# Optimization experiments

Hardware: AMD Instinct MI355X
Metric: run time of the kernel (lower is better)

Reference implementation:

```python
import jax, jax.numpy as jnp
import numpy as np

N = 8192          # batch_size == number of graph nodes
F1 = 64
F2 = 64
D_IN = F1 * F2    # 4096, = int(sqrt(in_feats))**2
D_OUT = 4096      # out_feats, must equal F1*F2 for the final reshape
ALPHA = 0.2       # LeakyReLU negative slope


def setup_inputs() -> dict:
    key = jax.random.key(0)
    k_x, k_w, k_a = jax.random.split(key, 3)
    x = jax.random.normal(k_x, (N, F1, F2), dtype=jnp.float32)
    # torch Linear weight layout: [out_feats, in_feats]; xavier-uniform-ish scale
    lim_w = float(np.sqrt(6.0 / (D_IN + D_OUT)) * np.sqrt(2.0))
    W = jax.random.uniform(k_w, (D_OUT, D_IN), dtype=jnp.float32, minval=-lim_w, maxval=lim_w)
    lim_a = float(np.sqrt(6.0 / (1 + 2 * D_OUT)))
    a = jax.random.uniform(k_a, (1, 2 * D_OUT), dtype=jnp.float32, minval=-lim_a, maxval=lim_a)
    return {"x": x, "W": W, "a": a}


def reference(x, W, a):
    b, f1, f2 = x.shape
    x_flat = x.reshape(b, f1 * f2)                 # [N, D_in]
    h = x_flat @ W.T                               # [N, D_out]
    # scores[i,j] = leakyrelu(cat(h_i, h_j) @ a.T) = leakyrelu(h_i.a1 + h_j.a2)
    a1 = a[0, :D_OUT]                              # [D_out]
    a2 = a[0, D_OUT:]                              # [D_out]
    s1 = h @ a1                                    # [N]
    s2 = h @ a2                                    # [N]
    e = s1[:, None] + s2[None, :]                  # [N, N]
    e = jnp.where(e > 0, e, ALPHA * e)             # LeakyReLU
    attention = jax.nn.softmax(e, axis=-1)         # [N, N]
    # dropout=0.0 (eval-mode / deterministic reference)
    out = attention @ h                            # [N, D_out]
    return out.reshape(b, f1, f2)
```

## Files before the change

### kernel.cpp

```cpp
#include <hip/hip_runtime.h>
#include <hip/hip_bf16.h>
#include <stdint.h>


typedef float  f32x4  __attribute__((ext_vector_type(4)));
typedef __bf16 bf16x8 __attribute__((ext_vector_type(8)));

#define AS1 __attribute__((address_space(1)))
#define AS3 __attribute__((address_space(3)))

constexpr int NB  = 8192;
constexpr int DF  = 4096;
constexpr int CH  = 64;
constexpr int NCH = NB / CH;

constexpr int GK  = DF;
constexpr int BKK = 64;
constexpr int NT2 = GK / BKK;

__device__ __forceinline__ uint16_t f2bf_u(float f) {
  union { float f; uint32_t u; } x; x.f = f;
  return (uint16_t)((x.u + 0x7FFFu + ((x.u >> 16) & 1u)) >> 16);
}
__device__ __forceinline__ float bfu2f(uint16_t v) {
  union { uint32_t u; float f; } x; x.u = ((uint32_t)v) << 16;
  return x.f;
}

__global__ __launch_bounds__(256) void cvt_f32_to_bf16(
    const float* __restrict__ in, uint16_t* __restrict__ out, int n4) {
  int idx = blockIdx.x * 256 + threadIdx.x;
  int stride = gridDim.x * 256;
  for (int i = idx; i < n4; i += stride) {
    float4 v = ((const float4*)in)[i];
    ushort4 o;
    o.x = f2bf_u(v.x); o.y = f2bf_u(v.y); o.z = f2bf_u(v.z); o.w = f2bf_u(v.w);
    ((ushort4*)out)[i] = o;
  }
}


#define STAGE_A(tt, half) do {                                                 \
  const uint16_t* g0_ = Ag + (size_t)((half) * 128) * GK + (size_t)(tt) * BKK; \
  uint32_t d_ = ((uint32_t)((tt) & 1)) * 32768u + (uint32_t)(half) * 8192u +   \
                (uint32_t)wave * 512u;                                         \
  __builtin_amdgcn_global_load_lds((const AS1 void*)g0_,                       \
      (AS3 void*)(lds + d_), 16, 0, 0);                                        \
  __builtin_amdgcn_global_load_lds((const AS1 void*)(g0_ + (size_t)64 * GK),   \
      (AS3 void*)(lds + d_ + 4096u), 16, 0, 0);                                \
} while (0)

#define STAGE_B(tt, half) do {                                                 \
  const uint16_t* g0_ = Bg + (size_t)((half) * 128) * GK + (size_t)(tt) * BKK; \
  uint32_t d_ = ((uint32_t)((tt) & 1)) * 32768u + 16384u +                     \
                (uint32_t)(half) * 8192u + (uint32_t)wave * 512u;              \
  __builtin_amdgcn_global_load_lds((const AS1 void*)g0_,                       \
      (AS3 void*)(lds + d_), 16, 0, 0);                                        \
  __builtin_amdgcn_global_load_lds((const AS1 void*)(g0_ + (size_t)64 * GK),   \
      (AS3 void*)(lds + d_ + 4096u), 16, 0, 0);                                \
} while (0)

#define LDA(mh) do {                                                           \
  _Pragma("unroll") for (int mf = 0; mf < 4; ++mf)                             \
    _Pragma("unroll") for (int ks = 0; ks < 2; ++ks)                           \
      aF[mf][ks] = *(const bf16x8*)(lds + bufo +                               \
          (uint32_t)(wm * 128 + (mh) * 64 + mf * 16 + lr) * 64u +              \
          (uint32_t)((ks * 32 + lg * 8) ^ swl));                               \
} while (0)

#define LDB(nh) do {                                                           \
  _Pragma("unroll") for (int nf = 0; nf < 2; ++nf)                             \
    _Pragma("unroll") for (int ks = 0; ks < 2; ++ks)                           \
      bF[nf][ks] = *(const bf16x8*)(lds + bufo + 16384u +                      \
          (uint32_t)(wn * 64 + (nh) * 32 + nf * 16 + lr) * 64u +               \
          (uint32_t)((ks * 32 + lg * 8) ^ swl));                               \
} while (0)

#define MMA(mh, nh) do {                                                       \
  _Pragma("unroll") for (int mf = 0; mf < 4; ++mf)                             \
    _Pragma("unroll") for (int nf = 0; nf < 2; ++nf)                           \
      _Pragma("unroll") for (int ks = 0; ks < 2; ++ks)                         \
        acc[(mh) * 4 + mf][(nh) * 2 + nf] =                                    \
            __builtin_amdgcn_mfma_f32_16x16x32_bf16(aF[mf][ks], bF[nf][ks],    \
                acc[(mh) * 4 + mf][(nh) * 2 + nf], 0, 0, 0);                   \
} while (0)

__global__ __launch_bounds__(512, 2) void gemm_nt_8phase(
    const uint16_t* __restrict__ A, const uint16_t* __restrict__ B,
    uint16_t* __restrict__ C) {
  __shared__ uint16_t lds[65536];

  const int tid  = threadIdx.x;
  const int wave = tid >> 6;
  const int lane = tid & 63;
  const int lr   = lane & 15;
  const int lg   = lane >> 4;
  const int wm   = wave >> 2;
  const int wn   = wave & 3;
  const int swl  = (lr & 7) << 3;

  const int bid = blockIdx.x;
  const int swz = (bid & 7) * 64 + (bid >> 3);
  const int bx  = swz & 15;
  const int by  = swz >> 4;
  const int rowBase = by * 256;
  const int colBase = bx * 256;

  const int sr  = tid >> 3;
  const int sch = (tid & 7) ^ (sr & 7);
  const uint16_t* Ag = A + (size_t)(rowBase + sr) * GK + sch * 8;
  const uint16_t* Bg = B + (size_t)(colBase + sr) * GK + sch * 8;

  f32x4 acc[8][4];
#pragma unroll
  for (int mf = 0; mf < 8; ++mf)
#pragma unroll
    for (int nf = 0; nf < 4; ++nf) acc[mf][nf] = (f32x4){0.f, 0.f, 0.f, 0.f};

  STAGE_A(0, 0);
  STAGE_B(0, 1);
  STAGE_A(0, 1);
  STAGE_B(0, 0);
  STAGE_A(1, 0);
  STAGE_B(1, 1);
  asm volatile("s_waitcnt vmcnt(4)" ::: "memory");
  __builtin_amdgcn_s_barrier();

  bf16x8 aF[4][2], bF[2][2];

  for (int t = 0; t < NT2; ++t) {
    const uint32_t bufo = ((uint32_t)(t & 1)) * 32768u;

    LDA(0); LDB(0);
    if (t + 1 < NT2) STAGE_A(t + 1, 1);
    __builtin_amdgcn_s_barrier();
    __builtin_amdgcn_s_setprio(1);
    MMA(0, 0);
    __builtin_amdgcn_s_setprio(0);
    __builtin_amdgcn_s_barrier();

    LDB(1);
    if (t + 1 < NT2) STAGE_B(t + 1, 0);
    __builtin_amdgcn_s_barrier();
    __builtin_amdgcn_s_setprio(1);
    MMA(0, 1);
    __builtin_amdgcn_s_setprio(0);
    __builtin_amdgcn_s_barrier();

    LDA(1);
    if (t + 2 < NT2) STAGE_A(t + 2, 0);
    __builtin_amdgcn_s_barrier();
    __builtin_amdgcn_s_setprio(1);
    MMA(1, 1);
    __builtin_amdgcn_s_setprio(0);
    __builtin_amdgcn_s_barrier();

    LDB(0);
    if (t + 2 < NT2) STAGE_B(t + 2, 1);
    __builtin_amdgcn_s_barrier();
    __builtin_amdgcn_s_setprio(1);
    MMA(1, 0);
    __builtin_amdgcn_s_setprio(0);
    if (t + 2 < NT2) {
      asm volatile("s_waitcnt vmcnt(4)" ::: "memory");
    } else if (t + 1 < NT2) {
      asm volatile("s_waitcnt vmcnt(0)" ::: "memory");
    }
    __builtin_amdgcn_s_barrier();
  }

  const int r0 = rowBase + wm * 128 + lg * 4;
  const int c0 = colBase + wn * 64 + lr;
#pragma unroll
  for (int mf = 0; mf < 8; ++mf)
#pragma unroll
    for (int nf = 0; nf < 4; ++nf)
#pragma unroll
      for (int e = 0; e < 4; ++e)
        C[(size_t)(r0 + mf * 16 + e) * (size_t)DF + (c0 + nf * 16)] =
            f2bf_u(acc[mf][nf][e]);
}

__global__ __launch_bounds__(256) void s12_kernel(
    const uint16_t* __restrict__ h, const float* __restrict__ a,
    float* __restrict__ s1, float* __restrict__ s2) {
  const int wave = threadIdx.x >> 6, lane = threadIdx.x & 63;
  const int row = blockIdx.x * 4 + wave;
  const uint32_t* hr = (const uint32_t*)(h + (size_t)row * DF);
  float d1 = 0.f, d2 = 0.f;
#pragma unroll 4
  for (int it = 0; it < DF / 128; it++) {
    int u = it * 64 + lane;
    uint32_t hv = hr[u];
    float lo = bfu2f((uint16_t)hv), hi = bfu2f((uint16_t)(hv >> 16));
    int k = 2 * u;
    d1 += a[k] * lo + a[k + 1] * hi;
    d2 += a[DF + k] * lo + a[DF + k + 1] * hi;
  }
  for (int off = 32; off > 0; off >>= 1) {
    d1 += __shfl_down(d1, off, 64);
    d2 += __shfl_down(d2, off, 64);
  }
  if (lane == 0) { s1[row] = d1; s2[row] = d2; }
}

__global__ __launch_bounds__(256) void rank_kernel(
    const float* __restrict__ s2, int* __restrict__ pi,
    float* __restrict__ s2sorted) {
  __shared__ float ld[NB];
  for (int idx = threadIdx.x; idx < NB; idx += 256) ld[idx] = s2[idx];
  __syncthreads();
  const int j = blockIdx.x * 256 + threadIdx.x;
  const float v = ld[j];
  int cnt = 0;
  for (int q = 0; q < NB / 4; q++) {
    float4 u = ((const float4*)ld)[q];
    int jj = q * 4;
    cnt += (u.x > v) || (u.x == v && (jj + 0) < j);
    cnt += (u.y > v) || (u.y == v && (jj + 1) < j);
    cnt += (u.z > v) || (u.z == v && (jj + 2) < j);
    cnt += (u.w > v) || (u.w == v && (jj + 3) < j);
  }
  pi[cnt] = j;
  s2sorted[cnt] = v;
}

__global__ __launch_bounds__(256) void count_kernel(
    const float* __restrict__ s1, const float* __restrict__ s2,
    int* __restrict__ ci) {
  __shared__ float ld[NB];
  for (int idx = threadIdx.x; idx < NB; idx += 256) ld[idx] = s2[idx];
  __syncthreads();
  const int i = blockIdx.x * 256 + threadIdx.x;
  const float thr = -s1[i];
  int cnt = 0;
  for (int q = 0; q < NB / 4; q++) {
    float4 u = ((const float4*)ld)[q];
    cnt += (u.x > thr) + (u.y > thr) + (u.z > thr) + (u.w > thr);
  }
  ci[i] = cnt;
}

__global__ __launch_bounds__(256) void scan_kernel(
    const float* __restrict__ s2sorted, float* __restrict__ Sb,
    float* __restrict__ Sc, float* __restrict__ wbg, float* __restrict__ wcg) {
  __shared__ float pb[256], pc[256];
  const int t = threadIdx.x;
  float sb = 0.f, sc = 0.f;
  for (int c = t * 32; c < t * 32 + 32; c++) {
    float s = s2sorted[c];
    float wb = __expf(0.2f * s), wc = __expf(s);
    wbg[c] = wb; wcg[c] = wc;
    sb += wb; sc += wc;
  }
  pb[t] = sb; pc[t] = sc;
  __syncthreads();
  if (t == 0) {
    float rb = 0.f, rc = 0.f;
    for (int q = 0; q < 256; q++) {
      float tb = pb[q], tc = pc[q];
      pb[q] = rb; pc[q] = rc;
      rb += tb; rc += tc;
    }
    Sb[0] = 0.f; Sc[0] = 0.f;
    Sb[NB] = rb; Sc[NB] = rc;
  }
  __syncthreads();
  float rb = pb[t], rc = pc[t];
  for (int c = t * 32; c < t * 32 + 32; c++) {
    rb += wbg[c]; rc += wcg[c];
    if (c + 1 < NB) { Sb[c + 1] = rb; Sc[c + 1] = rc; }
  }
}

__global__ __launch_bounds__(256) void zero_hist(int* __restrict__ hist) {
  int t = blockIdx.x * 256 + threadIdx.x;
  if (t <= NB) hist[t] = 0;
}

__global__ __launch_bounds__(256) void finalize_kernel(
    const float* __restrict__ s1, const int* __restrict__ ci,
    const float* __restrict__ Sb, const float* __restrict__ Sc,
    float* __restrict__ f1, float* __restrict__ f2, int* __restrict__ hist) {
  const int i = blockIdx.x * 256 + threadIdx.x;
  const float s1i = s1[i];
  const int c = ci[i];
  const float q1 = __expf(0.2f * s1i), q2 = __expf(s1i);
  const float l = q1 * (Sb[NB] - Sb[c]) + q2 * Sc[c];
  f1[i] = q1 / l;
  f2[i] = q2 / l;
  atomicAdd(&hist[c], 1);
}

__global__ __launch_bounds__(256) void bucket_scan(
    const int* __restrict__ hist, int* __restrict__ istart,
    int* __restrict__ cursor) {
  __shared__ int ps[256];
  const int t = threadIdx.x;
  const int lo = t * 33;
  const int hi = min(lo + 33, NB + 1);
  int s = 0;
  for (int b = lo; b < hi; b++) s += hist[b];
  ps[t] = s;
  __syncthreads();
  if (t == 0) {
    int r = 0;
    for (int q = 0; q < 256; q++) { int v = ps[q]; ps[q] = r; r += v; }
  }
  __syncthreads();
  int r = ps[t];
  for (int b = lo; b < hi; b++) { istart[b] = r; cursor[b] = r; r += hist[b]; }
  if (t == 255) istart[NB + 1] = r;
}

__global__ __launch_bounds__(256) void scatter_kernel(
    const int* __restrict__ ci, int* __restrict__ cursor,
    int* __restrict__ ilist) {
  const int i = blockIdx.x * 256 + threadIdx.x;
  const int b = ci[i];
  const int pos = atomicAdd(&cursor[b], 1);
  ilist[pos] = i;
}

__global__ __launch_bounds__(256) void pass1_kernel(
    const uint16_t* __restrict__ h, const int* __restrict__ pi,
    const float* __restrict__ wbg, const float* __restrict__ wcg,
    float* __restrict__ Bct, float* __restrict__ Cct) {
  __shared__ int   pj[CH];
  __shared__ float wb[CH], wc[CH];
  const int t  = threadIdx.x;
  const int cb = blockIdx.x;
  const int k  = blockIdx.y;
  if (t < CH) {
    int g = k * CH + t;
    pj[t] = pi[g]; wb[t] = wbg[g]; wc[t] = wcg[g];
  }
  __syncthreads();
  const int n0 = cb * 512 + t * 2;
  float b0 = 0.f, b1 = 0.f, c0 = 0.f, c1 = 0.f;
#pragma unroll 4
  for (int c = 0; c < CH; c++) {
    uint32_t hv = *(const uint32_t*)(h + (size_t)pj[c] * DF + n0);
    float h0 = bfu2f((uint16_t)hv), h1 = bfu2f((uint16_t)(hv >> 16));
    b0 += wb[c] * h0; b1 += wb[c] * h1;
    c0 += wc[c] * h0; c1 += wc[c] * h1;
  }
  *(float2*)(Bct + (size_t)k * DF + n0) = make_float2(b0, b1);
  *(float2*)(Cct + (size_t)k * DF + n0) = make_float2(c0, c1);
}

__global__ __launch_bounds__(256) void boff_kernel(
    const float* __restrict__ Bct, const float* __restrict__ Cct,
    float* __restrict__ Boff, float* __restrict__ Coff) {
  const int n = blockIdx.x * 256 + threadIdx.x;
  float ob = 0.f, oc = 0.f;
  for (int k = 0; k < NCH; k++) {
    Boff[(size_t)k * DF + n] = ob;
    Coff[(size_t)k * DF + n] = oc;
    ob += Bct[(size_t)k * DF + n];
    oc += Cct[(size_t)k * DF + n];
  }
  Boff[(size_t)NCH * DF + n] = ob;
  Coff[(size_t)NCH * DF + n] = oc;
}

__global__ __launch_bounds__(256) void pass2_kernel(
    const uint16_t* __restrict__ h, const int* __restrict__ pi,
    const float* __restrict__ wbg, const float* __restrict__ wcg,
    const float* __restrict__ Boff, const float* __restrict__ Coff,
    const int* __restrict__ istart, const int* __restrict__ ilist,
    const float* __restrict__ f1, const float* __restrict__ f2,
    float* __restrict__ out) {
  __shared__ int   pj[CH];
  __shared__ float wb[CH], wc[CH];
  __shared__ int   se[CH + 2];
  const int t  = threadIdx.x;
  const int cb = blockIdx.x;
  const int k  = blockIdx.y;
  if (t < CH) {
    int g = k * CH + t;
    pj[t] = pi[g]; wb[t] = wbg[g]; wc[t] = wcg[g];
  }
  if (t < CH + 2) se[t] = istart[k * CH + t];
  __syncthreads();
  const int n0 = cb * 512 + t * 2;
  const float2 An = *(const float2*)(Boff + (size_t)NCH * DF + n0);
  const float2 Bo = *(const float2*)(Boff + (size_t)k * DF + n0);
  const float2 Co = *(const float2*)(Coff + (size_t)k * DF + n0);
  float b0 = Bo.x, b1 = Bo.y, c0 = Co.x, c1 = Co.y;

  if (k == 0) {
    for (int idx = se[0]; idx < se[1]; idx++) {
      const int i = ilist[idx];
      const float fa = f1[i];
      *(float2*)(out + (size_t)i * DF + n0) = make_float2(fa * An.x, fa * An.y);
    }
  }
  for (int c = 0; c < CH; c++) {
    uint32_t hv = *(const uint32_t*)(h + (size_t)pj[c] * DF + n0);
    float h0 = bfu2f((uint16_t)hv), h1 = bfu2f((uint16_t)(hv >> 16));
    b0 += wb[c] * h0; b1 += wb[c] * h1;
    c0 += wc[c] * h0; c1 += wc[c] * h1;
    const int e0 = se[c + 1], e1 = se[c + 2];
    for (int idx = e0; idx < e1; idx++) {
      const int i = ilist[idx];
      const float fa = f1[i], fb = f2[i];
      float o0 = fa * (An.x - b0) + fb * c0;
      float o1 = fa * (An.y - b1) + fb * c1;
      *(float2*)(out + (size_t)i * DF + n0) = make_float2(o0, o1);
    }
  }
}

extern "C" void kernel_launch(void* const* d_in, const int* in_sizes, int n_in,
                              void* d_out, int out_size, void* d_ws, size_t ws_size,
                              hipStream_t stream) {
  const float* x = (const float*)d_in[0];
  const float* W = (const float*)d_in[1];
  const float* a = (const float*)d_in[2];
  float* out = (float*)d_out;

  char* ws = (char*)d_ws;
  uint16_t* h = (uint16_t*)ws;
  char* sm = ws + 67108864;
  float* s1       = (float*)(sm);
  float* s2       = (float*)(sm + 65536);
  float* s2sorted = (float*)(sm + 131072);
  int*   pi       = (int*)  (sm + 196608);
  int*   ci       = (int*)  (sm + 262144);
  float* Sb       = (float*)(sm + 327680);
  float* Sc       = (float*)(sm + 393216);
  float* wbg      = (float*)(sm + 458752);
  float* wcg      = (float*)(sm + 524288);
  float* f1       = (float*)(sm + 589824);
  float* f2       = (float*)(sm + 655360);
  int*   hist     = (int*)  (sm + 720896);
  int*   istart   = (int*)  (sm + 786432);
  int*   cursor   = (int*)  (sm + 851968);
  int*   ilist    = (int*)  (sm + 917504);
  float* Bct      = (float*)(sm + 1048576);
  float* Cct      = (float*)(sm + 3145728);
  float* Boff     = (float*)(sm + 5242880);
  float* Coff     = (float*)(sm + 7602176);
  char* base2 = ws + 67108864 + 10485760;
  uint16_t* xb = (uint16_t*)base2;
  uint16_t* Wb = (uint16_t*)(base2 + 67108864);

  cvt_f32_to_bf16<<<1024, 256, 0, stream>>>(x, xb, (NB * DF) / 4);
  cvt_f32_to_bf16<<<1024, 256, 0, stream>>>(W, Wb, (DF * DF) / 4);

  gemm_nt_8phase<<<(NB / 256) * (DF / 256), 512, 0, stream>>>(xb, Wb, h);

  zero_hist<<<33, 256, 0, stream>>>(hist);
  s12_kernel<<<NB / 4, 256, 0, stream>>>(h, a, s1, s2);
  rank_kernel<<<NB / 256, 256, 0, stream>>>(s2, pi, s2sorted);
  count_kernel<<<NB / 256, 256, 0, stream>>>(s1, s2, ci);
  scan_kernel<<<1, 256, 0, stream>>>(s2sorted, Sb, Sc, wbg, wcg);
  finalize_kernel<<<NB / 256, 256, 0, stream>>>(s1, ci, Sb, Sc, f1, f2, hist);
  bucket_scan<<<1, 256, 0, stream>>>(hist, istart, cursor);
  scatter_kernel<<<NB / 256, 256, 0, stream>>>(ci, cursor, ilist);

  pass1_kernel<<<dim3(DF / 512, NCH), 256, 0, stream>>>(h, pi, wbg, wcg, Bct, Cct);
  boff_kernel<<<DF / 256, 256, 0, stream>>>(Bct, Cct, Boff, Coff);
  pass2_kernel<<<dim3(DF / 512, NCH), 256, 0, stream>>>(
      h, pi, wbg, wcg, Boff, Coff, istart, ilist, f1, f2, out);
}
```

Measured before the change: 885.1 us.

## Simplify GEMM prefetch, vectorize pass kernels, parallelize prefix-offset scan

Three independent changes ship together. The GEMM main loop drops the 8-phase interleaved staging with priority hints and per-phase barriers: it now prefetches the whole next K-tile at the top of each iteration and waits once at the end. This also reorders the MFMA loop so ks is outermost. pass1 and pass2 process 4 columns per thread with 64-bit loads and float4 stores, halving the grid, and boff splits the 128-chunk prefix scan into 4 segments per column with a shared-memory combine to raise parallelism. The coarser GEMM pipeline may expose more load latency, and the halved pass grids cut the number of waves in flight.

```diff
diff --git a/kernel.cpp b/kernel.cpp
--- a/kernel.cpp
+++ b/kernel.cpp
@@ -77,15 +77,15 @@
 } while (0)
 
 #define MMA(mh, nh) do {                                                       \
-  _Pragma("unroll") for (int mf = 0; mf < 4; ++mf)                             \
-    _Pragma("unroll") for (int nf = 0; nf < 2; ++nf)                           \
-      _Pragma("unroll") for (int ks = 0; ks < 2; ++ks)                         \
+  _Pragma("unroll") for (int ks = 0; ks < 2; ++ks)                             \
+    _Pragma("unroll") for (int mf = 0; mf < 4; ++mf)                           \
+      _Pragma("unroll") for (int nf = 0; nf < 2; ++nf)                         \
         acc[(mh) * 4 + mf][(nh) * 2 + nf] =                                    \
             __builtin_amdgcn_mfma_f32_16x16x32_bf16(aF[mf][ks], bF[nf][ks],    \
                 acc[(mh) * 4 + mf][(nh) * 2 + nf], 0, 0, 0);                   \
 } while (0)
 
-__global__ __launch_bounds__(512, 2) void gemm_nt_8phase(
+__global__ __launch_bounds__(512, 2) void gemm_nt_async(
     const uint16_t* __restrict__ A, const uint16_t* __restrict__ B,
     uint16_t* __restrict__ C) {
   __shared__ uint16_t lds[65536];
@@ -118,12 +118,10 @@
     for (int nf = 0; nf < 4; ++nf) acc[mf][nf] = (f32x4){0.f, 0.f, 0.f, 0.f};
 
   STAGE_A(0, 0);
-  STAGE_B(0, 1);
   STAGE_A(0, 1);
   STAGE_B(0, 0);
-  STAGE_A(1, 0);
-  STAGE_B(1, 1);
-  asm volatile("s_waitcnt vmcnt(4)" ::: "memory");
+  STAGE_B(0, 1);
+  asm volatile("s_waitcnt vmcnt(0)" ::: "memory");
   __builtin_amdgcn_s_barrier();
 
   bf16x8 aF[4][2], bF[2][2];
@@ -131,42 +129,26 @@
   for (int t = 0; t < NT2; ++t) {
     const uint32_t bufo = ((uint32_t)(t & 1)) * 32768u;
 
+    if (t + 1 < NT2) {
+      STAGE_A(t + 1, 0);
+      STAGE_A(t + 1, 1);
+      STAGE_B(t + 1, 0);
+      STAGE_B(t + 1, 1);
+    }
+
     LDA(0); LDB(0);
-    if (t + 1 < NT2) STAGE_A(t + 1, 1);
-    __builtin_amdgcn_s_barrier();
-    __builtin_amdgcn_s_setprio(1);
     MMA(0, 0);
-    __builtin_amdgcn_s_setprio(0);
-    __builtin_amdgcn_s_barrier();
-
     LDB(1);
-    if (t + 1 < NT2) STAGE_B(t + 1, 0);
-    __builtin_amdgcn_s_barrier();
-    __builtin_amdgcn_s_setprio(1);
     MMA(0, 1);
-    __builtin_amdgcn_s_setprio(0);
-    __builtin_amdgcn_s_barrier();
-
     LDA(1);
-    if (t + 2 < NT2) STAGE_A(t + 2, 0);
-    __builtin_amdgcn_s_barrier();
-    __builtin_amdgcn_s_setprio(1);
     MMA(1, 1);
-    __builtin_amdgcn_s_setprio(0);
-    __builtin_amdgcn_s_barrier();
-
     LDB(0);
-    if (t + 2 < NT2) STAGE_B(t + 2, 1);
-    __builtin_amdgcn_s_barrier();
-    __builtin_amdgcn_s_setprio(1);
     MMA(1, 0);
-    __builtin_amdgcn_s_setprio(0);
-    if (t + 2 < NT2) {
-      asm volatile("s_waitcnt vmcnt(4)" ::: "memory");
-    } else if (t + 1 < NT2) {
+
+    if (t + 1 < NT2) {
       asm volatile("s_waitcnt vmcnt(0)" ::: "memory");
+      __builtin_amdgcn_s_barrier();
     }
-    __builtin_amdgcn_s_barrier();
   }
 
   const int r0 = rowBase + wm * 128 + lg * 4;
@@ -336,32 +318,55 @@
     pj[t] = pi[g]; wb[t] = wbg[g]; wc[t] = wcg[g];
   }
   __syncthreads();
-  const int n0 = cb * 512 + t * 2;
-  float b0 = 0.f, b1 = 0.f, c0 = 0.f, c1 = 0.f;
-#pragma unroll 4
+  const int n0 = cb * 1024 + t * 4;
+  float b0 = 0.f, b1 = 0.f, b2 = 0.f, b3 = 0.f;
+  float c0 = 0.f, c1 = 0.f, c2 = 0.f, c3 = 0.f;
+#pragma unroll 8
   for (int c = 0; c < CH; c++) {
-    uint32_t hv = *(const uint32_t*)(h + (size_t)pj[c] * DF + n0);
-    float h0 = bfu2f((uint16_t)hv), h1 = bfu2f((uint16_t)(hv >> 16));
-    b0 += wb[c] * h0; b1 += wb[c] * h1;
-    c0 += wc[c] * h0; c1 += wc[c] * h1;
-  }
-  *(float2*)(Bct + (size_t)k * DF + n0) = make_float2(b0, b1);
-  *(float2*)(Cct + (size_t)k * DF + n0) = make_float2(c0, c1);
+    uint2 hv = *(const uint2*)(h + (size_t)pj[c] * DF + n0);
+    float h0 = bfu2f((uint16_t)hv.x), h1 = bfu2f((uint16_t)(hv.x >> 16));
+    float h2 = bfu2f((uint16_t)hv.y), h3 = bfu2f((uint16_t)(hv.y >> 16));
+    float vb = wb[c], vc = wc[c];
+    b0 += vb * h0; b1 += vb * h1; b2 += vb * h2; b3 += vb * h3;
+    c0 += vc * h0; c1 += vc * h1; c2 += vc * h2; c3 += vc * h3;
+  }
+  *(float4*)(Bct + (size_t)k * DF + n0) = make_float4(b0, b1, b2, b3);
+  *(float4*)(Cct + (size_t)k * DF + n0) = make_float4(c0, c1, c2, c3);
 }
 
 __global__ __launch_bounds__(256) void boff_kernel(
     const float* __restrict__ Bct, const float* __restrict__ Cct,
     float* __restrict__ Boff, float* __restrict__ Coff) {
-  const int n = blockIdx.x * 256 + threadIdx.x;
-  float ob = 0.f, oc = 0.f;
-  for (int k = 0; k < NCH; k++) {
-    Boff[(size_t)k * DF + n] = ob;
-    Coff[(size_t)k * DF + n] = oc;
-    ob += Bct[(size_t)k * DF + n];
-    oc += Cct[(size_t)k * DF + n];
-  }
-  Boff[(size_t)NCH * DF + n] = ob;
-  Coff[(size_t)NCH * DF + n] = oc;
+  __shared__ float sB[4][64], sC[4][64];
+  const int t   = threadIdx.x;
+  const int cl  = t & 63;
+  const int seg = t >> 6;
+  const int col = blockIdx.x * 64 + cl;
+  float sb = 0.f, sc = 0.f;
+#pragma unroll 8
+  for (int u = 0; u < NCH / 4; u++) {
+    int kk = seg * (NCH / 4) + u;
+    sb += Bct[(size_t)kk * DF + col];
+    sc += Cct[(size_t)kk * DF + col];
+  }
+  sB[seg][cl] = sb; sC[seg][cl] = sc;
+  __syncthreads();
+  float rb = 0.f, rc = 0.f;
+#pragma unroll
+  for (int s = 0; s < 3; s++)
+    if (s < seg) { rb += sB[s][cl]; rc += sC[s][cl]; }
+#pragma unroll 4
+  for (int u = 0; u < NCH / 4; u++) {
+    int kk = seg * (NCH / 4) + u;
+    Boff[(size_t)kk * DF + col] = rb;
+    Coff[(size_t)kk * DF + col] = rc;
+    rb += Bct[(size_t)kk * DF + col];
+    rc += Cct[(size_t)kk * DF + col];
+  }
+  if (seg == 3) {
+    Boff[(size_t)NCH * DF + col] = rb;
+    Coff[(size_t)NCH * DF + col] = rc;
+  }
 }
 
 __global__ __launch_bounds__(256) void pass2_kernel(
@@ -383,31 +388,35 @@
   }
   if (t < CH + 2) se[t] = istart[k * CH + t];
   __syncthreads();
-  const int n0 = cb * 512 + t * 2;
-  const float2 An = *(const float2*)(Boff + (size_t)NCH * DF + n0);
-  const float2 Bo = *(const float2*)(Boff + (size_t)k * DF + n0);
-  const float2 Co = *(const float2*)(Coff + (size_t)k * DF + n0);
-  float b0 = Bo.x, b1 = Bo.y, c0 = Co.x, c1 = Co.y;
+  const int n0 = cb * 1024 + t * 4;
+  const float4 An = *(const float4*)(Boff + (size_t)NCH * DF + n0);
+  const float4 Bo = *(const float4*)(Boff + (size_t)k * DF + n0);
+  const float4 Co = *(const float4*)(Coff + (size_t)k * DF + n0);
+  float b0 = Bo.x, b1 = Bo.y, b2 = Bo.z, b3 = Bo.w;
+  float c0 = Co.x, c1 = Co.y, c2 = Co.z, c3 = Co.w;
 
   if (k == 0) {
     for (int idx = se[0]; idx < se[1]; idx++) {
       const int i = ilist[idx];
       const float fa = f1[i];
-      *(float2*)(out + (size_t)i * DF + n0) = make_float2(fa * An.x, fa * An.y);
+      *(float4*)(out + (size_t)i * DF + n0) =
+          make_float4(fa * An.x, fa * An.y, fa * An.z, fa * An.w);
     }
   }
   for (int c = 0; c < CH; c++) {
-    uint32_t hv = *(const uint32_t*)(h + (size_t)pj[c] * DF + n0);
-    float h0 = bfu2f((uint16_t)hv), h1 = bfu2f((uint16_t)(hv >> 16));
-    b0 += wb[c] * h0; b1 += wb[c] * h1;
-    c0 += wc[c] * h0; c1 += wc[c] * h1;
+    uint2 hv = *(const uint2*)(h + (size_t)pj[c] * DF + n0);
+    float h0 = bfu2f((uint16_t)hv.x), h1 = bfu2f((uint16_t)(hv.x >> 16));
+    float h2 = bfu2f((uint16_t)hv.y), h3 = bfu2f((uint16_t)(hv.y >> 16));
+    float vb = wb[c], vc = wc[c];
+    b0 += vb * h0; b1 += vb * h1; b2 += vb * h2; b3 += vb * h3;
+    c0 += vc * h0; c1 += vc * h1; c2 += vc * h2; c3 += vc * h3;
     const int e0 = se[c + 1], e1 = se[c + 2];
     for (int idx = e0; idx < e1; idx++) {
       const int i = ilist[idx];
       const float fa = f1[i], fb = f2[i];
-      float o0 = fa * (An.x - b0) + fb * c0;
-      float o1 = fa * (An.y - b1) + fb * c1;
-      *(float2*)(out + (size_t)i * DF + n0) = make_float2(o0, o1);
+      *(float4*)(out + (size_t)i * DF + n0) = make_float4(
+          fa * (An.x - b0) + fb * c0, fa * (An.y - b1) + fb * c1,
+          fa * (An.z - b2) + fb * c2, fa * (An.w - b3) + fb * c3);
     }
   }
 }
@@ -449,7 +458,7 @@
   cvt_f32_to_bf16<<<1024, 256, 0, stream>>>(x, xb, (NB * DF) / 4);
   cvt_f32_to_bf16<<<1024, 256, 0, stream>>>(W, Wb, (DF * DF) / 4);
 
-  gemm_nt_8phase<<<(NB / 256) * (DF / 256), 512, 0, stream>>>(xb, Wb, h);
+  gemm_nt_async<<<(NB / 256) * (DF / 256), 512, 0, stream>>>(xb, Wb, h);
 
   zero_hist<<<33, 256, 0, stream>>>(hist);
   s12_kernel<<<NB / 4, 256, 0, stream>>>(h, a, s1, s2);
@@ -460,8 +469,8 @@
   bucket_scan<<<1, 256, 0, stream>>>(hist, istart, cursor);
   scatter_kernel<<<NB / 256, 256, 0, stream>>>(ci, cursor, ilist);
 
-  pass1_kernel<<<dim3(DF / 512, NCH), 256, 0, stream>>>(h, pi, wbg, wcg, Bct, Cct);
-  boff_kernel<<<DF / 256, 256, 0, stream>>>(Bct, Cct, Boff, Coff);
-  pass2_kernel<<<dim3(DF / 512, NCH), 256, 0, stream>>>(
+  pass1_kernel<<<dim3(DF / 1024, NCH), 256, 0, stream>>>(h, pi, wbg, wcg, Bct, Cct);
+  boff_kernel<<<DF / 64, 256, 0, stream>>>(Bct, Cct, Boff, Coff);
+  pass2_kernel<<<dim3(DF / 1024, NCH), 256, 0, stream>>>(
       h, pi, wbg, wcg, Boff, Coff, istart, ilist, f1, f2, out);
 }
```

Result: no change. 897.7 us (+1.4%).
